# Kernel tuning notes

Hardware: AMD Instinct MI355X
Metric: run time of the kernel (lower is better)

Reference implementation:

```python
import jax, jax.numpy as jnp
import numpy as np

D_MODEL = 768

def setup_inputs() -> dict:
    key = jax.random.key(0)
    k1, k2, k3, k4 = jax.random.split(key, 4)
    x = jax.random.normal(k1, (2, 2048, D_MODEL), dtype=jnp.float32)
    w_qkv = jax.random.normal(k2, (3 * D_MODEL, D_MODEL), dtype=jnp.float32) * (1.0 / np.sqrt(D_MODEL))
    w_fc = jax.random.normal(k3, (D_MODEL, D_MODEL), dtype=jnp.float32) * (1.0 / np.sqrt(D_MODEL))
    b_fc = jax.random.normal(k4, (D_MODEL,), dtype=jnp.float32) * 0.01
    return {"x": x, "w_qkv": w_qkv, "w_fc": w_fc, "b_fc": b_fc, "n_head": 12}


def reference(x, w_qkv, w_fc, b_fc, n_head):
    b, n, d = x.shape
    h = int(n_head)
    d_k = d // h
    temperature = float(d_k) ** 0.5  # NOTE: source MULTIPLIES by sqrt(d_k)
    qkv = x @ w_qkv.T                                  # [b, n, 3d] (qkv_bias=False)
    # rearrange 'b n (qkv d h) -> qkv b h n d' : split order is (qkv, d_k, h)
    qkv = qkv.reshape(b, n, 3, d_k, h).transpose(2, 0, 4, 1, 3)  # [3, b, h, n, d_k]
    q, k, v = qkv[0], qkv[1], qkv[2]
    attn = jnp.einsum('bhid,bhjd->bhij', q, k) * temperature      # [b, h, n, n]
    attn = jax.nn.softmax(attn, axis=-1)                           # dropout p=0 -> identity
    out = jnp.einsum('bhij,bhjd->bhid', attn, v)                   # [b, h, n, d_k]
    out = out.transpose(0, 2, 1, 3).reshape(b, n, d)               # 'b h n d -> b n (h d)'
    out = out @ w_fc.T + b_fc                                      # fc (dropout p=0 -> identity)
    return out
```

## Files before the change

### kernel.cpp

```cpp
#include <hip/hip_runtime.h>
#include <stdint.h>

typedef float f32x4 __attribute__((ext_vector_type(4)));
typedef _Float16 f16;
typedef f16 f16x8 __attribute__((ext_vector_type(8)));
typedef f16 f16x4 __attribute__((ext_vector_type(4)));
typedef f16 f16x2 __attribute__((ext_vector_type(2)));

#define MFMA16(a, b, c) __builtin_amdgcn_mfma_f32_16x16x32_f16((a), (b), (c), 0, 0, 0)

__device__ __forceinline__ float fexp2(float x) {
    return __builtin_amdgcn_exp2f(x);
}
__device__ __forceinline__ f16x2 cvt_pk_f16(float a, float b) {
    auto p = __builtin_amdgcn_cvt_pkrtz(a, b);
    return *(f16x2*)&p;
}

typedef __attribute__((address_space(1))) const uint32_t gu32;
typedef __attribute__((address_space(3))) uint32_t lu32;
__device__ __forceinline__ void gload_lds16(const void* g, void* l) {
    __builtin_amdgcn_global_load_lds((gu32*)g, (lu32*)l, 16, 0, 0);
}

__device__ __forceinline__ size_t kv_elem(int bh, int n, int d) {
    const int kt = n >> 6, row = n & 63;
    return ((size_t)(bh * 32 + kt)) * 4096 + row * 64 + (((d >> 3) ^ (row & 7)) << 3) + (d & 7);
}

__global__ void split_inputs(const float* __restrict__ X, const float* __restrict__ Wq,
                             const float* __restrict__ Wf,
                             f16* __restrict__ Xh, f16* __restrict__ Xl,
                             f16* __restrict__ Wh, f16* __restrict__ Wfb) {
    const int tid = blockIdx.x * 256 + threadIdx.x;
    if (tid < 393216) {
        const float* s = X + (size_t)tid * 8;
        f16 hi[8], lo[8];
#pragma unroll
        for (int j = 0; j < 8; j += 4) {
            f32x4 v = *(const f32x4*)(s + j);
#pragma unroll
            for (int q = 0; q < 4; ++q) {
                f16 h = (f16)v[q];
                hi[j + q] = h;
                lo[j + q] = (f16)(v[q] - (float)h);
            }
        }
        *(f16x8*)(Xh + (size_t)tid * 8) = *(f16x8*)hi;
        *(f16x8*)(Xl + (size_t)tid * 8) = *(f16x8*)lo;
    } else if (tid < 614400) {
        const int t2 = tid - 393216;
        const int row = t2 / 96;
        const int k = (t2 % 96) * 8;
        const int c = row / 768;
        const int rem = row - c * 768;
        const int d = rem / 12;
        const int h2 = rem - d * 12;
        const int cp = c * 768 + h2 * 64 + d;
        const float* s = Wq + (size_t)row * 768 + k;
        f16 hi[8];
#pragma unroll
        for (int j = 0; j < 8; j += 4) {
            f32x4 v = *(const f32x4*)(s + j);
#pragma unroll
            for (int q = 0; q < 4; ++q) hi[j + q] = (f16)v[q];
        }
        *(f16x8*)(Wh + (size_t)cp * 768 + k) = *(f16x8*)hi;
    } else {
        const int t2 = tid - 614400;
        const float* s = Wf + (size_t)t2 * 8;
        f16 hi[8];
#pragma unroll
        for (int j = 0; j < 8; j += 4) {
            f32x4 v = *(const f32x4*)(s + j);
#pragma unroll
            for (int q = 0; q < 4; ++q) hi[j + q] = (f16)v[q];
        }
        *(f16x8*)(Wfb + (size_t)t2 * 8) = *(f16x8*)hi;
    }
}

__global__ __launch_bounds__(256) void qkv_gemm(
    const f16* __restrict__ Xh, const f16* __restrict__ Xl,
    const f16* __restrict__ Wh,
    f16* __restrict__ Qh, f16* __restrict__ Ql,
    f16* __restrict__ Khg, f16* __restrict__ VTg) {
    __shared__ f16 Ah[2][4096], Al[2][4096], Bh[2][4096];
    const int t = threadIdx.x;
    const int lane = t & 63, wv = t >> 6;
    const int wm = (wv >> 1) * 64, wn = (wv & 1) * 64;
    const int r = lane & 15, g = lane >> 4;
    const int bm = blockIdx.x, bn = blockIdx.y;
    const bool full = (bn < 12);

    const int lrow = lane >> 2;
    const int lk = (lane & 3) * 8;

    f32x4 acc[4][4];
#pragma unroll
    for (int i = 0; i < 4; ++i)
#pragma unroll
        for (int j = 0; j < 4; ++j) acc[i][j] = (f32x4)0.0f;

    auto stage = [&](int ksi, int buf) {
#pragma unroll
        for (int hh = 0; hh < 2; ++hh) {
            const int ii = wv * 2 + hh;
            const int grow = ii * 16 + lrow;
            const size_t ga = (size_t)(bm * 128 + grow) * 768 + ksi * 32 + lk;
            const size_t gb = (size_t)(bn * 128 + grow) * 768 + ksi * 32 + lk;
            gload_lds16(Xh + ga, &Ah[buf][ii * 512]);
            gload_lds16(Wh + gb, &Bh[buf][ii * 512]);
            if (full) gload_lds16(Xl + ga, &Al[buf][ii * 512]);
        }
    };

    stage(0, 0);
    int cur = 0;
    for (int i = 0; i < 24; ++i) {
        __syncthreads();
        if (i < 23) stage(i + 1, cur ^ 1);

        f16x8 a_h[4], b[4];
#pragma unroll
        for (int mf = 0; mf < 4; ++mf) a_h[mf] = *(f16x8*)&Ah[cur][(wm + mf * 16 + r) * 32 + g * 8];
#pragma unroll
        for (int nf = 0; nf < 4; ++nf) b[nf] = *(f16x8*)&Bh[cur][(wn + nf * 16 + r) * 32 + g * 8];
        if (full) {
            f16x8 a_l[4];
#pragma unroll
            for (int mf = 0; mf < 4; ++mf) a_l[mf] = *(f16x8*)&Al[cur][(wm + mf * 16 + r) * 32 + g * 8];
#pragma unroll
            for (int mf = 0; mf < 4; ++mf)
#pragma unroll
                for (int nf = 0; nf < 4; ++nf) {
                    acc[mf][nf] = MFMA16(a_h[mf], b[nf], acc[mf][nf]);
                    acc[mf][nf] = MFMA16(a_l[mf], b[nf], acc[mf][nf]);
                }
        } else {
#pragma unroll
            for (int mf = 0; mf < 4; ++mf)
#pragma unroll
                for (int nf = 0; nf < 4; ++nf)
                    acc[mf][nf] = MFMA16(a_h[mf], b[nf], acc[mf][nf]);
        }
        cur ^= 1;
    }

    const int comp = bn / 6;
#pragma unroll
    for (int mf = 0; mf < 4; ++mf)
#pragma unroll
        for (int nf = 0; nf < 4; ++nf) {
            const int col = bn * 128 + wn + nf * 16 + r;
            const int h = (col >> 6) % 12;
            const int d = col & 63;
            if (comp == 2) {
                const int row0 = bm * 128 + wm + mf * 16 + g * 4;
                const int b2 = row0 >> 11, n = row0 & 2047;
                const int bh = b2 * 12 + h;
                const int tile = bh * 32 + (n >> 6);
                const int kvl = n & 63;
                const int kc = kvl >> 5, u = (kvl >> 4) & 1, gl = (kvl >> 2) & 3;
                f16 o4[4];
#pragma unroll
                for (int v = 0; v < 4; ++v) o4[v] = (f16)acc[mf][nf][v];
                *(f16x4*)&VTg[(size_t)tile * 4096 + kc * 2048 + d * 32 +
                              ((gl ^ ((d >> 1) & 3)) << 3) + u * 4] = *(f16x4*)o4;
            } else {
#pragma unroll
                for (int v = 0; v < 4; ++v) {
                    const int row = bm * 128 + wm + mf * 16 + g * 4 + v;
                    const int b2 = row >> 11, n = row & 2047;
                    const int bh = b2 * 12 + h;
                    float val = acc[mf][nf][v];
                    if (comp == 0) {
                        const size_t dest = ((size_t)bh * 2048 + n) * 64 + d;
                        val *= 11.5415603629f;
                        f16 hi = (f16)val;
                        Qh[dest] = hi;
                        Ql[dest] = (f16)(val - (float)hi);
                    } else {
                        Khg[kv_elem(bh, n, d)] = (f16)val;
                    }
                }
            }
        }
}

__global__ __launch_bounds__(256) void attn_partial(
    const f16* __restrict__ Qh, const f16* __restrict__ Ql,
    const f16* __restrict__ Khg, const f16* __restrict__ VTg,
    f16* __restrict__ OP, float* __restrict__ Mst, float* __restrict__ Lst) {
    const int t = threadIdx.x;
    const int lane = t & 63, wv = t >> 6;
    const int r = lane & 15, g = lane >> 4;
    const int bid = blockIdx.x;
    const int qb = bid & 15;
    const int pb = bid >> 4;
    const int part = pb % 3;
    const int bh = pb / 3;
    const size_t headoff = (size_t)bh * 2048 * 64;
    const int q0w = qb * 128 + wv * 32;
    const int kt0 = part * 11;
    const int nt = (part == 2) ? 10 : 11;

    const int ksw0 = ((g ^ (r & 7)) << 3);
    const int ksw1 = (((4 + g) ^ (r & 7)) << 3);
    const int vsw = ((g ^ ((r >> 1) & 3)) << 3);

    f16x8 qh[2][2], ql[2][2];
#pragma unroll
    for (int qf = 0; qf < 2; ++qf)
#pragma unroll
        for (int kc = 0; kc < 2; ++kc) {
            const size_t off = headoff + (size_t)(q0w + qf * 16 + r) * 64 + kc * 32 + g * 8;
            qh[qf][kc] = *(const f16x8*)(Qh + off);
            ql[qf][kc] = *(const f16x8*)(Ql + off);
        }

    f32x4 o_accT[2][4], lacc[2];
    float m_run[2] = {-1e30f, -1e30f};
#pragma unroll
    for (int qf = 0; qf < 2; ++qf) {
        lacc[qf] = (f32x4)0.0f;
#pragma unroll
        for (int df = 0; df < 4; ++df) o_accT[qf][df] = (f32x4)0.0f;
    }
    const f16x8 ones8 = {(f16)1.0f, (f16)1.0f, (f16)1.0f, (f16)1.0f,
                         (f16)1.0f, (f16)1.0f, (f16)1.0f, (f16)1.0f};

    for (int i = 0; i < nt; ++i) {
        const int kt = kt0 + i;
        const f16* Kt = Khg + (size_t)(bh * 32 + kt) * 4096;
        const f16* Vt = VTg + (size_t)(bh * 32 + kt) * 4096;

        f16x8 ka0[4], ka1[4];
#pragma unroll
        for (int cf = 0; cf < 4; ++cf) {
            ka0[cf] = *(const f16x8*)(Kt + (cf * 16 + r) * 64 + ksw0);
            ka1[cf] = *(const f16x8*)(Kt + (cf * 16 + r) * 64 + ksw1);
        }

        f32x4 s[2][4];
#pragma unroll
        for (int qf = 0; qf < 2; ++qf)
#pragma unroll
            for (int cf = 0; cf < 4; ++cf) s[qf][cf] = (f32x4)0.0f;
#pragma unroll
        for (int cf = 0; cf < 4; ++cf)
#pragma unroll
            for (int qf = 0; qf < 2; ++qf) {
                s[qf][cf] = MFMA16(ka0[cf], qh[qf][0], s[qf][cf]);
                s[qf][cf] = MFMA16(ka0[cf], ql[qf][0], s[qf][cf]);
                s[qf][cf] = MFMA16(ka1[cf], qh[qf][1], s[qf][cf]);
                s[qf][cf] = MFMA16(ka1[cf], ql[qf][1], s[qf][cf]);
            }

        f16x8 vb[2][4];
#pragma unroll
        for (int kc = 0; kc < 2; ++kc)
#pragma unroll
            for (int df = 0; df < 4; ++df)
                vb[kc][df] = *(const f16x8*)(Vt + kc * 2048 + (df * 16 + r) * 32 + vsw);

        f16x8 pa[2][2];
#pragma unroll
        for (int qf = 0; qf < 2; ++qf) {
            float mx = -1e30f;
#pragma unroll
            for (int cf = 0; cf < 4; ++cf)
#pragma unroll
                for (int v = 0; v < 4; ++v) mx = fmaxf(mx, s[qf][cf][v]);
            mx = fmaxf(mx, __shfl_xor(mx, 16));
            mx = fmaxf(mx, __shfl_xor(mx, 32));
            if (__any(mx - m_run[qf] > 8.0f)) {
                const float mn = fmaxf(m_run[qf], mx);
                const float sc = fexp2(m_run[qf] - mn);
                m_run[qf] = mn;
                lacc[qf] *= sc;
#pragma unroll
                for (int df = 0; df < 4; ++df) o_accT[qf][df] *= sc;
            }
            const float mr = m_run[qf];
            union { f16x8 v8; f16x2 v2[4]; } pk[2];
#pragma unroll
            for (int cf = 0; cf < 4; ++cf) {
                const float p0 = fexp2(s[qf][cf][0] - mr);
                const float p1 = fexp2(s[qf][cf][1] - mr);
                const float p2 = fexp2(s[qf][cf][2] - mr);
                const float p3 = fexp2(s[qf][cf][3] - mr);
                pk[cf >> 1].v2[(cf & 1) * 2]     = cvt_pk_f16(p0, p1);
                pk[cf >> 1].v2[(cf & 1) * 2 + 1] = cvt_pk_f16(p2, p3);
            }
            pa[qf][0] = pk[0].v8;
            pa[qf][1] = pk[1].v8;
        }

#pragma unroll
        for (int kc = 0; kc < 2; ++kc) {
#pragma unroll
            for (int df = 0; df < 4; ++df)
#pragma unroll
                for (int qf = 0; qf < 2; ++qf)
                    o_accT[qf][df] = MFMA16(vb[kc][df], pa[qf][kc], o_accT[qf][df]);
#pragma unroll
            for (int qf = 0; qf < 2; ++qf)
                lacc[qf] = MFMA16(ones8, pa[qf][kc], lacc[qf]);
        }
    }

#pragma unroll
    for (int qf = 0; qf < 2; ++qf) {
        const int n = q0w + qf * 16 + r;
        const float lq = lacc[qf][0];
        if (g == 0) {
            Mst[pb * 2048 + n] = m_run[qf];
            Lst[pb * 2048 + n] = lq;
        }
        const float linv = 1.0f / lq;
#pragma unroll
        for (int df = 0; df < 4; ++df) {
            f16 o4[4];
#pragma unroll
            for (int v = 0; v < 4; ++v) o4[v] = (f16)(o_accT[qf][df][v] * linv);
            *(f16x4*)&OP[((size_t)pb * 2048 + n) * 64 + df * 16 + g * 4] = *(f16x4*)o4;
        }
    }
}

__global__ void attn_combine(const f16* __restrict__ OP, const float* __restrict__ Mst,
                             const float* __restrict__ Lst, f16* __restrict__ AO) {
    const int tid = blockIdx.x * 256 + threadIdx.x;
    const int d4 = (tid & 15) * 4;
    const int pr = tid >> 4;
    const int bh = pr >> 11, n = pr & 2047;
    const int i0 = (bh * 3) * 2048 + n;
    const float m0 = Mst[i0], m1 = Mst[i0 + 2048], m2 = Mst[i0 + 4096];
    const float m = fmaxf(fmaxf(m0, m1), m2);
    const float c0 = __builtin_amdgcn_exp2f(m0 - m) * Lst[i0];
    const float c1 = __builtin_amdgcn_exp2f(m1 - m) * Lst[i0 + 2048];
    const float c2 = __builtin_amdgcn_exp2f(m2 - m) * Lst[i0 + 4096];
    const float inv = 1.0f / (c0 + c1 + c2);
    f16x4 o0 = *(const f16x4*)(OP + (size_t)i0 * 64 + d4);
    f16x4 o1 = *(const f16x4*)(OP + (size_t)(i0 + 2048) * 64 + d4);
    f16x4 o2 = *(const f16x4*)(OP + (size_t)(i0 + 4096) * 64 + d4);
    const int b = bh / 12, h = bh - b * 12;
    f16 out[4];
#pragma unroll
    for (int j = 0; j < 4; ++j)
        out[j] = (f16)((c0 * (float)o0[j] + c1 * (float)o1[j] + c2 * (float)o2[j]) * inv);
    *(f16x4*)(AO + ((size_t)(b * 2048 + n)) * 768 + h * 64 + d4) = *(f16x4*)out;
}

__global__ __launch_bounds__(256) void fc_gemm(const f16* __restrict__ A,
                                               const f16* __restrict__ Wfb,
                                               const float* __restrict__ bias,
                                               float* __restrict__ OUT) {
    __shared__ f16 As[64 * 64], Bs[64 * 64];
    const int t = threadIdx.x;
    const int lane = t & 63, wv = t >> 6;
    const int wm = (wv >> 1) * 32, wn = (wv & 1) * 32;
    const int r = lane & 15, g = lane >> 4;
    const int bm = blockIdx.x, bn = blockIdx.y;

    f32x4 acc[2][2];
#pragma unroll
    for (int i = 0; i < 2; ++i)
#pragma unroll
        for (int j = 0; j < 2; ++j) acc[i][j] = (f32x4)0.0f;

    const int srow = t >> 2;
    const int ssg = (t & 3) * 2;

    for (int ks = 0; ks < 768; ks += 64) {
        const f16* as = A + (size_t)(bm * 64 + srow) * 768 + ks;
        const f16* bs = Wfb + (size_t)(bn * 64 + srow) * 768 + ks;
#pragma unroll
        for (int u = 0; u < 2; ++u) {
            const int sg = ssg + u;
            const int dst = srow * 64 + ((sg ^ (srow & 7)) << 3);
            *(f16x8*)&As[dst] = *(const f16x8*)(as + sg * 8);
            *(f16x8*)&Bs[dst] = *(const f16x8*)(bs + sg * 8);
        }
        __syncthreads();

#pragma unroll
        for (int kc = 0; kc < 2; ++kc) {
            f16x8 a[2], b[2];
#pragma unroll
            for (int mf = 0; mf < 2; ++mf) {
                const int row = wm + mf * 16 + r;
                a[mf] = *(f16x8*)&As[row * 64 + (((kc * 4 + g) ^ (row & 7)) << 3)];
            }
#pragma unroll
            for (int nf = 0; nf < 2; ++nf) {
                const int row = wn + nf * 16 + r;
                b[nf] = *(f16x8*)&Bs[row * 64 + (((kc * 4 + g) ^ (row & 7)) << 3)];
            }
#pragma unroll
            for (int mf = 0; mf < 2; ++mf)
#pragma unroll
                for (int nf = 0; nf < 2; ++nf)
                    acc[mf][nf] = MFMA16(a[mf], b[nf], acc[mf][nf]);
        }
        __syncthreads();
    }

#pragma unroll
    for (int nf = 0; nf < 2; ++nf) {
        const int col = bn * 64 + wn + nf * 16 + r;
        const float bv = bias[col];
#pragma unroll
        for (int mf = 0; mf < 2; ++mf) {
            const int row = bm * 64 + wm + mf * 16 + g * 4;
#pragma unroll
            for (int v = 0; v < 4; ++v)
                OUT[(size_t)(row + v) * 768 + col] = acc[mf][nf][v] + bv;
        }
    }
}

extern "C" void kernel_launch(void* const* d_in, const int* in_sizes, int n_in,
                              void* d_out, int out_size, void* d_ws, size_t ws_size,
                              hipStream_t stream) {
    (void)in_sizes; (void)n_in; (void)out_size; (void)ws_size;
    const float* x     = (const float*)d_in[0];
    const float* w_qkv = (const float*)d_in[1];
    const float* w_fc  = (const float*)d_in[2];
    const float* b_fc  = (const float*)d_in[3];
    float* out = (float*)d_out;

    char* ws = (char*)d_ws;
    f16* Xh  = (f16*)ws;
    f16* Xl  = Xh + 3145728;
    f16* Qh  = Xl + 3145728;
    f16* Ql  = Qh + 3145728;
    f16* Khg = Ql + 3145728;
    f16* VTg = Khg + 3145728;
    f16* AO  = VTg + 3145728;
    f16* Wh  = AO + 3145728;
    f16* Wfb = Wh + 1769472;
    float* Mst = (float*)(Wfb + 589824);
    float* Lst = Mst + 147456;
    f16* OP  = (f16*)(Lst + 147456);

    split_inputs<<<2688, 256, 0, stream>>>(x, w_qkv, w_fc, Xh, Xl, Wh, Wfb);
    qkv_gemm<<<dim3(32, 18), 256, 0, stream>>>(Xh, Xl, Wh, Qh, Ql, Khg, VTg);
    attn_partial<<<1152, 256, 0, stream>>>(Qh, Ql, Khg, VTg, OP, Mst, Lst);
    attn_combine<<<3072, 256, 0, stream>>>(OP, Mst, Lst, AO);
    fc_gemm<<<dim3(64, 12), 256, 0, stream>>>(AO, Wfb, b_fc, out);
}
```

Before: 135.5 us.

## Fuse split-KV attention combine into FC GEMM A-tile load

Removes the separate attn_combine kernel and the AO intermediate buffer. The FC GEMM now merges the three partial attention outputs with their max/sum statistics while staging each A tile into LDS. It also rewrites the row-max reduction in attention as a tree of three-input max operations, so the compiler can emit max3 instructions. This saves one kernel launch and a write and read of AO, but each of the 12 column blocks now redoes the combine and reads three partial rows per A element.

```diff
diff --git a/kernel.cpp b/kernel.cpp
--- a/kernel.cpp
+++ b/kernel.cpp
@@ -15,6 +15,9 @@
 __device__ __forceinline__ f16x2 cvt_pk_f16(float a, float b) {
     auto p = __builtin_amdgcn_cvt_pkrtz(a, b);
     return *(f16x2*)&p;
+}
+__device__ __forceinline__ float max3f(float a, float b, float c) {
+    return fmaxf(fmaxf(a, b), c);
 }
 
 typedef __attribute__((address_space(1))) const uint32_t gu32;
@@ -267,11 +270,12 @@
         f16x8 pa[2][2];
 #pragma unroll
         for (int qf = 0; qf < 2; ++qf) {
-            float mx = -1e30f;
-#pragma unroll
-            for (int cf = 0; cf < 4; ++cf)
-#pragma unroll
-                for (int v = 0; v < 4; ++v) mx = fmaxf(mx, s[qf][cf][v]);
+            const float t0 = max3f(s[qf][0][0], s[qf][0][1], s[qf][0][2]);
+            const float t1 = max3f(s[qf][0][3], s[qf][1][0], s[qf][1][1]);
+            const float t2 = max3f(s[qf][1][2], s[qf][1][3], s[qf][2][0]);
+            const float t3 = max3f(s[qf][2][1], s[qf][2][2], s[qf][2][3]);
+            const float t4 = max3f(s[qf][3][0], s[qf][3][1], s[qf][3][2]);
+            float mx = fmaxf(max3f(t0, t1, t2), max3f(t3, t4, s[qf][3][3]));
             mx = fmaxf(mx, __shfl_xor(mx, 16));
             mx = fmaxf(mx, __shfl_xor(mx, 32));
             if (__any(mx - m_run[qf] > 8.0f)) {
@@ -329,34 +333,10 @@
     }
 }
 
-__global__ void attn_combine(const f16* __restrict__ OP, const float* __restrict__ Mst,
-                             const float* __restrict__ Lst, f16* __restrict__ AO) {
-    const int tid = blockIdx.x * 256 + threadIdx.x;
-    const int d4 = (tid & 15) * 4;
-    const int pr = tid >> 4;
-    const int bh = pr >> 11, n = pr & 2047;
-    const int i0 = (bh * 3) * 2048 + n;
-    const float m0 = Mst[i0], m1 = Mst[i0 + 2048], m2 = Mst[i0 + 4096];
-    const float m = fmaxf(fmaxf(m0, m1), m2);
-    const float c0 = __builtin_amdgcn_exp2f(m0 - m) * Lst[i0];
-    const float c1 = __builtin_amdgcn_exp2f(m1 - m) * Lst[i0 + 2048];
-    const float c2 = __builtin_amdgcn_exp2f(m2 - m) * Lst[i0 + 4096];
-    const float inv = 1.0f / (c0 + c1 + c2);
-    f16x4 o0 = *(const f16x4*)(OP + (size_t)i0 * 64 + d4);
-    f16x4 o1 = *(const f16x4*)(OP + (size_t)(i0 + 2048) * 64 + d4);
-    f16x4 o2 = *(const f16x4*)(OP + (size_t)(i0 + 4096) * 64 + d4);
-    const int b = bh / 12, h = bh - b * 12;
-    f16 out[4];
-#pragma unroll
-    for (int j = 0; j < 4; ++j)
-        out[j] = (f16)((c0 * (float)o0[j] + c1 * (float)o1[j] + c2 * (float)o2[j]) * inv);
-    *(f16x4*)(AO + ((size_t)(b * 2048 + n)) * 768 + h * 64 + d4) = *(f16x4*)out;
-}
-
-__global__ __launch_bounds__(256) void fc_gemm(const f16* __restrict__ A,
-                                               const f16* __restrict__ Wfb,
-                                               const float* __restrict__ bias,
-                                               float* __restrict__ OUT) {
+__global__ __launch_bounds__(256) void fc_gemm(
+    const f16* __restrict__ OP, const float* __restrict__ Mst,
+    const float* __restrict__ Lst, const f16* __restrict__ Wfb,
+    const float* __restrict__ bias, float* __restrict__ OUT) {
     __shared__ f16 As[64 * 64], Bs[64 * 64];
     const int t = threadIdx.x;
     const int lane = t & 63, wv = t >> 6;
@@ -373,14 +353,35 @@
     const int srow = t >> 2;
     const int ssg = (t & 3) * 2;
 
+    const int arow = bm * 64 + srow;
+    const int b2 = arow >> 11, n = arow & 2047;
+
     for (int ks = 0; ks < 768; ks += 64) {
-        const f16* as = A + (size_t)(bm * 64 + srow) * 768 + ks;
+        const int h = ks >> 6;
+        const int bh = b2 * 12 + h;
+        const size_t i0 = (size_t)(bh * 3) * 2048 + n;
+        const float m0 = Mst[i0], m1 = Mst[i0 + 2048], m2 = Mst[i0 + 4096];
+        const float m = max3f(m0, m1, m2);
+        const float c0 = fexp2(m0 - m) * Lst[i0];
+        const float c1 = fexp2(m1 - m) * Lst[i0 + 2048];
+        const float c2 = fexp2(m2 - m) * Lst[i0 + 4096];
+        const float inv = 1.0f / (c0 + c1 + c2);
+        const float w0 = c0 * inv, w1 = c1 * inv, w2 = c2 * inv;
+
         const f16* bs = Wfb + (size_t)(bn * 64 + srow) * 768 + ks;
 #pragma unroll
         for (int u = 0; u < 2; ++u) {
             const int sg = ssg + u;
+            const int d0 = sg * 8;
             const int dst = srow * 64 + ((sg ^ (srow & 7)) << 3);
-            *(f16x8*)&As[dst] = *(const f16x8*)(as + sg * 8);
+            f16x8 o0 = *(const f16x8*)(OP + i0 * 64 + d0);
+            f16x8 o1 = *(const f16x8*)(OP + (i0 + 2048) * 64 + d0);
+            f16x8 o2 = *(const f16x8*)(OP + (i0 + 4096) * 64 + d0);
+            f16 av[8];
+#pragma unroll
+            for (int j = 0; j < 8; ++j)
+                av[j] = (f16)(w0 * (float)o0[j] + w1 * (float)o1[j] + w2 * (float)o2[j]);
+            *(f16x8*)&As[dst] = *(f16x8*)av;
             *(f16x8*)&Bs[dst] = *(const f16x8*)(bs + sg * 8);
         }
         __syncthreads();
@@ -438,8 +439,7 @@
     f16* Ql  = Qh + 3145728;
     f16* Khg = Ql + 3145728;
     f16* VTg = Khg + 3145728;
-    f16* AO  = VTg + 3145728;
-    f16* Wh  = AO + 3145728;
+    f16* Wh  = VTg + 3145728;
     f16* Wfb = Wh + 1769472;
     float* Mst = (float*)(Wfb + 589824);
     float* Lst = Mst + 147456;
@@ -448,6 +448,5 @@
     split_inputs<<<2688, 256, 0, stream>>>(x, w_qkv, w_fc, Xh, Xl, Wh, Wfb);
     qkv_gemm<<<dim3(32, 18), 256, 0, stream>>>(Xh, Xl, Wh, Qh, Ql, Khg, VTg);
     attn_partial<<<1152, 256, 0, stream>>>(Qh, Ql, Khg, VTg, OP, Mst, Lst);
-    attn_combine<<<3072, 256, 0, stream>>>(OP, Mst, Lst, AO);
-    fc_gemm<<<dim3(64, 12), 256, 0, stream>>>(AO, Wfb, b_fc, out);
-}
+    fc_gemm<<<dim3(64, 12), 256, 0, stream>>>(OP, Mst, Lst, Wfb, b_fc, out);
+}
```

Result: slower. 139.5 us (+2.9%).
